# Performance work log

Hardware: AMD Instinct MI355X
Metric: run time of the kernel (lower is better)

## Reference

```python
import jax, jax.numpy as jnp
import numpy as np

B, S, E, H = 2, 2048, 1024, 16
D = E // H  # head_dim = 64


def setup_inputs() -> dict:
    key = jax.random.key(0)
    k1, k2, k3 = jax.random.split(key, 3)
    scale_in = 1.0 / np.sqrt(E)
    return {
        "x": jax.random.normal(k1, (B, S, E), dtype=jnp.float32),
        "W_attn": jax.random.normal(k2, (E, 3 * E), dtype=jnp.float32) * scale_in,
        "b_attn": jnp.zeros((3 * E,), dtype=jnp.float32),
        "W_proj": jax.random.normal(k3, (E, E), dtype=jnp.float32) * scale_in,
        "b_proj": jnp.zeros((E,), dtype=jnp.float32),
    }


def reference(x, W_attn, b_attn, W_proj, b_proj):
    # c_attn: fused QKV projection  [B,S,E] -> [B,S,3E]
    qkv = x @ W_attn + b_attn
    q, k, v = jnp.split(qkv, 3, axis=-1)
    # split heads -> [B,S,H,D]
    q = q.reshape(B, S, H, D)
    k = k.reshape(B, S, H, D)
    v = v.reshape(B, S, H, D)
    # scaled dot-product attention (no causal mask in the source module)
    scores = jnp.einsum("bqhd,bkhd->bhqk", q, k) / jnp.sqrt(jnp.float32(D))
    attn = jax.nn.softmax(scores, axis=-1)  # attn_dropout is identity in eval
    y = jnp.einsum("bhqk,bkhd->bqhd", attn, v).reshape(B, S, E)
    # c_proj; resid_dropout is identity in eval
    return y @ W_proj + b_proj
```

## Files before the change

kernel.cpp:

```cpp
#include <hip/hip_runtime.h>
#include <stdint.h>

#define NB 2
#define NS 2048
#define NE 1024
#define NH 16
#define ND 64
#define NE3 3072
#define NBS 4096

typedef _Float16 half8 __attribute__((ext_vector_type(8)));
typedef float f32x4 __attribute__((ext_vector_type(4)));

__device__ __forceinline__ void gload16(const void* g, void* l) {
  __builtin_amdgcn_global_load_lds(
      (__attribute__((address_space(1))) void*)const_cast<void*>(g),
      (__attribute__((address_space(3))) void*)l, 16, 0, 0);
}

__global__ void k_cvt16(const float* __restrict__ src, _Float16* __restrict__ dst, int n8) {
  int i = blockIdx.x * blockDim.x + threadIdx.x;
  if (i >= n8) return;
  const float4* s = (const float4*)src + (size_t)i * 2;
  float4 a = s[0], b = s[1];
  half8 o;
  o[0]=(_Float16)a.x; o[1]=(_Float16)a.y; o[2]=(_Float16)a.z; o[3]=(_Float16)a.w;
  o[4]=(_Float16)b.x; o[5]=(_Float16)b.y; o[6]=(_Float16)b.z; o[7]=(_Float16)b.w;
  *((half8*)dst + i) = o;
}

__global__ void k_cvtT(const float* __restrict__ src, _Float16* __restrict__ dst, int K, int N) {
  __shared__ _Float16 tile[64][72];
  int n0 = blockIdx.x * 64, k0 = blockIdx.y * 64;
  int t = threadIdx.x;
  int kk = t >> 2, nc = (t & 3) << 4;
  const float* sp = src + (size_t)(k0 + kk) * N + n0 + nc;
#pragma unroll
  for (int j = 0; j < 16; j += 4) {
    float4 v = *(const float4*)(sp + j);
    tile[kk][nc + j + 0] = (_Float16)v.x;
    tile[kk][nc + j + 1] = (_Float16)v.y;
    tile[kk][nc + j + 2] = (_Float16)v.z;
    tile[kk][nc + j + 3] = (_Float16)v.w;
  }
  __syncthreads();
  int nn = t >> 2, kc = (t & 3) << 4;
  half8 o0, o1;
#pragma unroll
  for (int j = 0; j < 8; ++j) { o0[j] = tile[kc + j][nn]; o1[j] = tile[kc + 8 + j][nn]; }
  _Float16* op = dst + (size_t)(n0 + nn) * K + k0 + kc;
  *(half8*)op = o0;
  *(half8*)(op + 8) = o1;
}

template <int OUT_HALF>
__global__ __launch_bounds__(256, 2)
void k_gemm(const _Float16* __restrict__ A, const _Float16* __restrict__ Bt,
            const float* __restrict__ bias, void* __restrict__ Cv,
            int M, int N, int K) {
  __shared__ _Float16 As[128 * 32];
  __shared__ _Float16 Bs[128 * 32];
  const int nwg = gridDim.x * gridDim.y;
  const int d = blockIdx.y * gridDim.x + blockIdx.x;
  const int lid = (d & 7) * (nwg >> 3) + (d >> 3);
  const int bx = lid % gridDim.x, by = lid / gridDim.x;
  const int m0 = by * 128, n0 = bx * 128;
  const int t = threadIdx.x, l = t & 63, w = t >> 6;
  const int wr = w >> 1, wc = w & 1;
  const int srow = l >> 2;
  const int sk = (l & 3) << 3;
  f32x4 acc[4][4] = {};
  for (int kt = 0; kt < K; kt += 32) {
    __syncthreads();
#pragma unroll
    for (int i = 0; i < 2; ++i) {
      int rb = (i * 4 + w) * 16;
      gload16(A + (size_t)(m0 + rb + srow) * K + kt + sk, (char*)As + (i * 4 + w) * 1024);
      gload16(Bt + (size_t)(n0 + rb + srow) * K + kt + sk, (char*)Bs + (i * 4 + w) * 1024);
    }
    __syncthreads();
    half8 a[4], b[4];
#pragma unroll
    for (int i = 0; i < 4; ++i)
      a[i] = *(const half8*)(As + (wr * 64 + i * 16 + (l & 15)) * 32 + ((l >> 4) << 3));
#pragma unroll
    for (int j = 0; j < 4; ++j)
      b[j] = *(const half8*)(Bs + (wc * 64 + j * 16 + (l & 15)) * 32 + ((l >> 4) << 3));
#pragma unroll
    for (int i = 0; i < 4; ++i)
#pragma unroll
      for (int j = 0; j < 4; ++j)
        acc[i][j] = __builtin_amdgcn_mfma_f32_16x16x32_f16(a[i], b[j], acc[i][j], 0, 0, 0);
  }
  float bv[4];
#pragma unroll
  for (int j = 0; j < 4; ++j) bv[j] = bias[n0 + wc * 64 + j * 16 + (l & 15)];
#pragma unroll
  for (int i = 0; i < 4; ++i) {
    int row0 = m0 + wr * 64 + i * 16 + ((l >> 4) << 2);
#pragma unroll
    for (int j = 0; j < 4; ++j) {
      int col = n0 + wc * 64 + j * 16 + (l & 15);
#pragma unroll
      for (int r = 0; r < 4; ++r) {
        float v = acc[i][j][r] + bv[j];
        if (OUT_HALF)
          ((_Float16*)Cv)[(size_t)(row0 + r) * N + col] = (_Float16)v;
        else
          ((float*)Cv)[(size_t)(row0 + r) * N + col] = v;
      }
    }
  }
}

__global__ void k_vt(const _Float16* __restrict__ qkv, _Float16* __restrict__ Vt) {
  __shared__ _Float16 tile[64][72];
  int s0 = blockIdx.x * 64;
  int bh = blockIdx.y, b = bh >> 4, h = bh & 15;
  int t = threadIdx.x;
  int ss = t >> 2, dc = (t & 3) << 4;
  const _Float16* sp = qkv + (size_t)(b * NS + s0 + ss) * NE3 + 2 * NE + h * ND + dc;
  half8 v0 = *(const half8*)sp, v1 = *(const half8*)(sp + 8);
#pragma unroll
  for (int j = 0; j < 8; ++j) { tile[ss][dc + j] = v0[j]; tile[ss][dc + 8 + j] = v1[j]; }
  __syncthreads();
  int d = t >> 2, sc = (t & 3) << 4;
  half8 o0, o1;
#pragma unroll
  for (int j = 0; j < 8; ++j) { o0[j] = tile[sc + j][d]; o1[j] = tile[sc + 8 + j][d]; }
  _Float16* op = Vt + (size_t)(bh * ND + d) * NS + s0 + sc;
  *(half8*)op = o0;
  *(half8*)(op + 8) = o1;
}

__global__ __launch_bounds__(256, 4)
void k_attn(const _Float16* __restrict__ qkv, const _Float16* __restrict__ Vt,
            _Float16* __restrict__ Y) {
  __shared__ _Float16 Kb[2][64 * 64];
  __shared__ _Float16 Vb[2][64 * 64];
  __shared__ _Float16 Pb[64 * 64];
  const int dly = blockIdx.y * 32 + blockIdx.x;
  const int lid = (dly & 7) * 128 + (dly >> 3);
  const int bh = lid >> 5, qb = lid & 31;
  const int q0 = qb * 64;
  const int b = bh >> 4, h = bh & 15;
  const int t = threadIdx.x, l = t & 63, w = t >> 6;
  const float cexp = 0.125f * 1.44269504088896340736f;

  half8 qf[2];
  {
    const _Float16* qp = qkv + (size_t)(b * NS + q0 + w * 16 + (l & 15)) * NE3 + h * ND + ((l >> 4) << 3);
    qf[0] = *(const half8*)qp;
    qf[1] = *(const half8*)(qp + 32);
  }

  f32x4 Oa[4] = {};
  f32x4 Osum = {};
  half8 ones;
#pragma unroll
  for (int j = 0; j < 8; ++j) ones[j] = (_Float16)1.0f;

  const int row8 = l >> 3;
  const int d0s_base = (l & 7) << 3;

#define STAGE_KV(KT, BUF)                                                            \
  {                                                                                  \
    _Pragma("unroll")                                                                \
    for (int i = 0; i < 2; ++i) {                                                    \
      int ci = w * 2 + i;                                                            \
      int row = ci * 8 + row8;                                                       \
      int d0s = d0s_base ^ ((row & 7) << 3);                                         \
      gload16(qkv + (size_t)(b * NS + (KT) * 64 + row) * NE3 + NE + h * ND + d0s,    \
              (char*)&Kb[BUF][0] + ci * 1024);                                       \
      gload16(Vt + (size_t)(bh * ND + row) * NS + (KT) * 64 + d0s,                   \
              (char*)&Vb[BUF][0] + ci * 1024);                                       \
    }                                                                                \
  }

  STAGE_KV(0, 0);
  __syncthreads();

  for (int kt = 0; kt < NS / 64; ++kt) {
    const int cur = kt & 1;
    if (kt + 1 < NS / 64) STAGE_KV(kt + 1, cur ^ 1);

    f32x4 sa[4] = {};
#pragma unroll
    for (int fc = 0; fc < 4; ++fc) {
      int key = fc * 16 + (l & 15);
#pragma unroll
      for (int ks = 0; ks < 2; ++ks) {
        half8 kf = *(const half8*)((char*)&Kb[cur][0] + key * 128 +
                                   ((ks * 64 + ((l >> 4) << 4)) ^ ((key & 7) << 4)));
        sa[fc] = __builtin_amdgcn_mfma_f32_16x16x32_f16(qf[ks], kf, sa[fc], 0, 0, 0);
      }
    }

#pragma unroll
    for (int r = 0; r < 4; ++r) {
      float p0 = __builtin_amdgcn_exp2f(sa[0][r] * cexp);
      float p1 = __builtin_amdgcn_exp2f(sa[1][r] * cexp);
      float p2 = __builtin_amdgcn_exp2f(sa[2][r] * cexp);
      float p3 = __builtin_amdgcn_exp2f(sa[3][r] * cexp);
      int q = w * 16 + ((l >> 4) << 2) + r;
      char* prow = (char*)Pb + q * 128;
      int kb = (l & 15);
      int sz = (q & 7) << 4;
      *(_Float16*)(prow + (((kb + 0) * 2) ^ sz)) = (_Float16)p0;
      *(_Float16*)(prow + (((kb + 16) * 2) ^ sz)) = (_Float16)p1;
      *(_Float16*)(prow + (((kb + 32) * 2) ^ sz)) = (_Float16)p2;
      *(_Float16*)(prow + (((kb + 48) * 2) ^ sz)) = (_Float16)p3;
    }

    asm volatile("s_waitcnt lgkmcnt(0)" ::: "memory");
    __builtin_amdgcn_sched_barrier(0);

#pragma unroll
    for (int ks = 0; ks < 2; ++ks) {
      int qp_ = w * 16 + (l & 15);
      half8 pf = *(const half8*)((char*)Pb + qp_ * 128 +
                                 ((ks * 64 + ((l >> 4) << 4)) ^ ((qp_ & 7) << 4)));
      Osum = __builtin_amdgcn_mfma_f32_16x16x32_f16(pf, ones, Osum, 0, 0, 0);
#pragma unroll
      for (int fc = 0; fc < 4; ++fc) {
        int dd = fc * 16 + (l & 15);
        half8 vf = *(const half8*)((char*)&Vb[cur][0] + dd * 128 +
                                   ((ks * 64 + ((l >> 4) << 4)) ^ ((dd & 7) << 4)));
        Oa[fc] = __builtin_amdgcn_mfma_f32_16x16x32_f16(pf, vf, Oa[fc], 0, 0, 0);
      }
    }
    __syncthreads();
  }

#pragma unroll
  for (int r = 0; r < 4; ++r) {
    int q = q0 + w * 16 + ((l >> 4) << 2) + r;
    float inv = 1.0f / Osum[r];
#pragma unroll
    for (int fc = 0; fc < 4; ++fc) {
      int dd = fc * 16 + (l & 15);
      Y[(size_t)(b * NS + q) * NE + h * ND + dd] = (_Float16)(Oa[fc][r] * inv);
    }
  }
}

extern "C" void kernel_launch(void* const* d_in, const int* in_sizes, int n_in,
                              void* d_out, int out_size, void* d_ws, size_t ws_size,
                              hipStream_t stream) {
  (void)in_sizes; (void)n_in; (void)out_size; (void)ws_size;
  const float* x      = (const float*)d_in[0];
  const float* W_attn = (const float*)d_in[1];
  const float* b_attn = (const float*)d_in[2];
  const float* W_proj = (const float*)d_in[3];
  const float* b_proj = (const float*)d_in[4];
  char* ws = (char*)d_ws;
  const size_t MB = 1024 * 1024;
  _Float16* qkvb = (_Float16*)(ws);
  _Float16* WaT  = (_Float16*)(ws + 24 * MB);
  _Float16* WpT  = (_Float16*)(ws + 30 * MB);
  _Float16* xb   = (_Float16*)(ws + 32 * MB);
  _Float16* Vt   = (_Float16*)(ws + 40 * MB);
  _Float16* yb   = (_Float16*)(ws + 32 * MB);

  k_cvt16<<<dim3(2048), dim3(256), 0, stream>>>(x, xb, NBS * NE / 8);
  k_cvtT<<<dim3(48, 16), dim3(256), 0, stream>>>(W_attn, WaT, NE, NE3);
  k_cvtT<<<dim3(16, 16), dim3(256), 0, stream>>>(W_proj, WpT, NE, NE);
  k_gemm<1><<<dim3(NE3 / 128, NBS / 128), dim3(256), 0, stream>>>(xb, WaT, b_attn, (void*)qkvb, NBS, NE3, NE);
  k_vt<<<dim3(NS / 64, NB * NH), dim3(256), 0, stream>>>(qkvb, Vt);
  k_attn<<<dim3(NS / 64, NB * NH), dim3(256), 0, stream>>>(qkvb, Vt, yb);
  k_gemm<0><<<dim3(NE / 128, NBS / 128), dim3(256), 0, stream>>>(yb, WpT, b_proj, d_out, NBS, NE, NE);
}
```

Measured before the change: 141.5 us.

## Double attention query tile to 128 rows per block for K/V reuse

Each attention block now handles 128 query rows instead of 64, with each wave computing two 16-row query subtiles against the same K/V tiles in shared memory. This halves the number of blocks and the total K/V global loads and LDS staging per query, and reuses each K and V fragment read for two MFMAs. In exchange it uses more registers and a larger P buffer, lowers launch bounds occupancy to 2, and launches 512 blocks instead of 1024, which may hurt latency hiding.

Measured after the change: 140.0 us. No clear change (-1.0%).

```diff
diff --git a/kernel.cpp b/kernel.cpp
--- a/kernel.cpp
+++ b/kernel.cpp
@@ -133,29 +133,30 @@
   *(half8*)(op + 8) = o1;
 }
 
-__global__ __launch_bounds__(256, 4)
+__global__ __launch_bounds__(256, 2)
 void k_attn(const _Float16* __restrict__ qkv, const _Float16* __restrict__ Vt,
             _Float16* __restrict__ Y) {
   __shared__ _Float16 Kb[2][64 * 64];
   __shared__ _Float16 Vb[2][64 * 64];
-  __shared__ _Float16 Pb[64 * 64];
-  const int dly = blockIdx.y * 32 + blockIdx.x;
-  const int lid = (dly & 7) * 128 + (dly >> 3);
-  const int bh = lid >> 5, qb = lid & 31;
-  const int q0 = qb * 64;
+  __shared__ _Float16 Pb[128 * 64];
+  const int dly = blockIdx.y * gridDim.x + blockIdx.x;
+  const int lid = (dly & 7) * 64 + (dly >> 3);
+  const int bh = lid >> 4, qb = lid & 15;
+  const int q0 = qb * 128;
   const int b = bh >> 4, h = bh & 15;
   const int t = threadIdx.x, l = t & 63, w = t >> 6;
   const float cexp = 0.125f * 1.44269504088896340736f;
 
-  half8 qf[2];
-  {
-    const _Float16* qp = qkv + (size_t)(b * NS + q0 + w * 16 + (l & 15)) * NE3 + h * ND + ((l >> 4) << 3);
-    qf[0] = *(const half8*)qp;
-    qf[1] = *(const half8*)(qp + 32);
-  }
-
-  f32x4 Oa[4] = {};
-  f32x4 Osum = {};
+  half8 qf[2][2];
+#pragma unroll
+  for (int m = 0; m < 2; ++m) {
+    const _Float16* qp = qkv + (size_t)(b * NS + q0 + w * 32 + m * 16 + (l & 15)) * NE3 + h * ND + ((l >> 4) << 3);
+    qf[m][0] = *(const half8*)qp;
+    qf[m][1] = *(const half8*)(qp + 32);
+  }
+
+  f32x4 Oa[2][4] = {};
+  f32x4 Osum[2] = {};
   half8 ones;
 #pragma unroll
   for (int j = 0; j < 8; ++j) ones[j] = (_Float16)1.0f;
@@ -184,7 +185,7 @@
     const int cur = kt & 1;
     if (kt + 1 < NS / 64) STAGE_KV(kt + 1, cur ^ 1);
 
-    f32x4 sa[4] = {};
+    f32x4 sa[2][4] = {};
 #pragma unroll
     for (int fc = 0; fc < 4; ++fc) {
       int key = fc * 16 + (l & 15);
@@ -192,24 +193,28 @@
       for (int ks = 0; ks < 2; ++ks) {
         half8 kf = *(const half8*)((char*)&Kb[cur][0] + key * 128 +
                                    ((ks * 64 + ((l >> 4) << 4)) ^ ((key & 7) << 4)));
-        sa[fc] = __builtin_amdgcn_mfma_f32_16x16x32_f16(qf[ks], kf, sa[fc], 0, 0, 0);
-      }
-    }
-
-#pragma unroll
-    for (int r = 0; r < 4; ++r) {
-      float p0 = __builtin_amdgcn_exp2f(sa[0][r] * cexp);
-      float p1 = __builtin_amdgcn_exp2f(sa[1][r] * cexp);
-      float p2 = __builtin_amdgcn_exp2f(sa[2][r] * cexp);
-      float p3 = __builtin_amdgcn_exp2f(sa[3][r] * cexp);
-      int q = w * 16 + ((l >> 4) << 2) + r;
-      char* prow = (char*)Pb + q * 128;
-      int kb = (l & 15);
-      int sz = (q & 7) << 4;
-      *(_Float16*)(prow + (((kb + 0) * 2) ^ sz)) = (_Float16)p0;
-      *(_Float16*)(prow + (((kb + 16) * 2) ^ sz)) = (_Float16)p1;
-      *(_Float16*)(prow + (((kb + 32) * 2) ^ sz)) = (_Float16)p2;
-      *(_Float16*)(prow + (((kb + 48) * 2) ^ sz)) = (_Float16)p3;
+        sa[0][fc] = __builtin_amdgcn_mfma_f32_16x16x32_f16(qf[0][ks], kf, sa[0][fc], 0, 0, 0);
+        sa[1][fc] = __builtin_amdgcn_mfma_f32_16x16x32_f16(qf[1][ks], kf, sa[1][fc], 0, 0, 0);
+      }
+    }
+
+#pragma unroll
+    for (int m = 0; m < 2; ++m) {
+#pragma unroll
+      for (int r = 0; r < 4; ++r) {
+        float p0 = __builtin_amdgcn_exp2f(sa[m][0][r] * cexp);
+        float p1 = __builtin_amdgcn_exp2f(sa[m][1][r] * cexp);
+        float p2 = __builtin_amdgcn_exp2f(sa[m][2][r] * cexp);
+        float p3 = __builtin_amdgcn_exp2f(sa[m][3][r] * cexp);
+        int q = w * 32 + m * 16 + ((l >> 4) << 2) + r;
+        char* prow = (char*)Pb + q * 128;
+        int kb = (l & 15);
+        int sz = (q & 7) << 4;
+        *(_Float16*)(prow + (((kb + 0) * 2) ^ sz)) = (_Float16)p0;
+        *(_Float16*)(prow + (((kb + 16) * 2) ^ sz)) = (_Float16)p1;
+        *(_Float16*)(prow + (((kb + 32) * 2) ^ sz)) = (_Float16)p2;
+        *(_Float16*)(prow + (((kb + 48) * 2) ^ sz)) = (_Float16)p3;
+      }
     }
 
     asm volatile("s_waitcnt lgkmcnt(0)" ::: "memory");
@@ -217,29 +222,37 @@
 
 #pragma unroll
     for (int ks = 0; ks < 2; ++ks) {
-      int qp_ = w * 16 + (l & 15);
-      half8 pf = *(const half8*)((char*)Pb + qp_ * 128 +
-                                 ((ks * 64 + ((l >> 4) << 4)) ^ ((qp_ & 7) << 4)));
-      Osum = __builtin_amdgcn_mfma_f32_16x16x32_f16(pf, ones, Osum, 0, 0, 0);
+      half8 pf[2];
+#pragma unroll
+      for (int m = 0; m < 2; ++m) {
+        int qp_ = w * 32 + m * 16 + (l & 15);
+        pf[m] = *(const half8*)((char*)Pb + qp_ * 128 +
+                                ((ks * 64 + ((l >> 4) << 4)) ^ ((qp_ & 7) << 4)));
+        Osum[m] = __builtin_amdgcn_mfma_f32_16x16x32_f16(pf[m], ones, Osum[m], 0, 0, 0);
+      }
 #pragma unroll
       for (int fc = 0; fc < 4; ++fc) {
         int dd = fc * 16 + (l & 15);
         half8 vf = *(const half8*)((char*)&Vb[cur][0] + dd * 128 +
                                    ((ks * 64 + ((l >> 4) << 4)) ^ ((dd & 7) << 4)));
-        Oa[fc] = __builtin_amdgcn_mfma_f32_16x16x32_f16(pf, vf, Oa[fc], 0, 0, 0);
+        Oa[0][fc] = __builtin_amdgcn_mfma_f32_16x16x32_f16(pf[0], vf, Oa[0][fc], 0, 0, 0);
+        Oa[1][fc] = __builtin_amdgcn_mfma_f32_16x16x32_f16(pf[1], vf, Oa[1][fc], 0, 0, 0);
       }
     }
     __syncthreads();
   }
 
 #pragma unroll
-  for (int r = 0; r < 4; ++r) {
-    int q = q0 + w * 16 + ((l >> 4) << 2) + r;
-    float inv = 1.0f / Osum[r];
-#pragma unroll
-    for (int fc = 0; fc < 4; ++fc) {
-      int dd = fc * 16 + (l & 15);
-      Y[(size_t)(b * NS + q) * NE + h * ND + dd] = (_Float16)(Oa[fc][r] * inv);
+  for (int m = 0; m < 2; ++m) {
+#pragma unroll
+    for (int r = 0; r < 4; ++r) {
+      int q = q0 + w * 32 + m * 16 + ((l >> 4) << 2) + r;
+      float inv = 1.0f / Osum[m][r];
+#pragma unroll
+      for (int fc = 0; fc < 4; ++fc) {
+        int dd = fc * 16 + (l & 15);
+        Y[(size_t)(b * NS + q) * NE + h * ND + dd] = (_Float16)(Oa[m][fc][r] * inv);
+      }
     }
   }
 }
@@ -267,6 +280,6 @@
   k_cvtT<<<dim3(16, 16), dim3(256), 0, stream>>>(W_proj, WpT, NE, NE);
   k_gemm<1><<<dim3(NE3 / 128, NBS / 128), dim3(256), 0, stream>>>(xb, WaT, b_attn, (void*)qkvb, NBS, NE3, NE);
   k_vt<<<dim3(NS / 64, NB * NH), dim3(256), 0, stream>>>(qkvb, Vt);
-  k_attn<<<dim3(NS / 64, NB * NH), dim3(256), 0, stream>>>(qkvb, Vt, yb);
+  k_attn<<<dim3(NS / 128, NB * NH), dim3(256), 0, stream>>>(qkvb, Vt, yb);
   k_gemm<0><<<dim3(NE / 128, NBS / 128), dim3(256), 0, stream>>>(yb, WpT, b_proj, d_out, NBS, NE, NE);
 }
```
